# Performance work log

Measured on AMD Instinct MI355X. Metric: run time of the kernel, lower is better.

Reference implementation:

```python
import jax, jax.numpy as jnp
import numpy as np

L, N, E, H = 2048, 4, 1024, 8


def setup_inputs() -> dict:
    key = jax.random.key(0)
    ks = jax.random.split(key, 5)
    s = 0.02
    x = jax.random.normal(ks[0], (L, N, E), dtype=jnp.float32)
    Wqkv = jax.random.normal(ks[1], (H, 3 * E, E), dtype=jnp.float32) * s
    bqkv = jnp.zeros((H, 3 * E), dtype=jnp.float32)
    Wo = jax.random.normal(ks[2], (H, E, E), dtype=jnp.float32) * s
    bo = jnp.zeros((H, E), dtype=jnp.float32)
    return {"x": x, "Wqkv": Wqkv, "bqkv": bqkv, "Wo": Wo, "bo": bo}


def reference(x, Wqkv, bqkv, Wo, bo):
    # x: [L, N, E]; each of H independent single-head attentions over full E,
    # outputs summed across heads (as in the torch module).
    scale = 1.0 / jnp.sqrt(jnp.asarray(E, dtype=x.dtype))
    # joint QKV projection per head: [H, L, N, 3E]
    qkv = jnp.einsum("lne,hfe->hlnf", x, Wqkv) + bqkv[:, None, None, :]
    q, k, v = jnp.split(qkv, 3, axis=-1)  # each [H, L, N, E]
    # scores over sequence: [H, N, L, L]
    scores = jnp.einsum("hlne,hmne->hnlm", q * scale, k)
    attn = jax.nn.softmax(scores, axis=-1)
    ctx = jnp.einsum("hnlm,hmne->hlne", attn, v)  # [H, L, N, E]
    out = jnp.einsum("hlne,hfe->hlnf", ctx, Wo) + bo[:, None, None, :]
    return out.sum(axis=0)  # [L, N, E]
```

## Files before the change

### kernel.cpp

```cpp
#include <hip/hip_runtime.h>

typedef __bf16 bf16;
typedef __bf16 bf16x4 __attribute__((ext_vector_type(4)));
typedef __bf16 bf16x8 __attribute__((ext_vector_type(8)));
typedef float f32x4 __attribute__((ext_vector_type(4)));
typedef unsigned int u32;
typedef unsigned short u16;

#define CL 2048
#define CN 4
#define CE 1024
#define CH 8

__device__ __forceinline__ void gload16(const bf16* g, bf16x8* l) {
  __builtin_amdgcn_global_load_lds((const __attribute__((address_space(1))) void*)g,
                                   (__attribute__((address_space(3))) void*)l, 16, 0, 0);
}

template<int BN>
__device__ __forceinline__ void gemm_mainloop256(
    const bf16* __restrict__ Abase, const bf16* __restrict__ Bbase,
    int lda, int ldb, int nk, f32x4 (&acc)[8][BN / 64])
{
  constexpr int BJ = BN / 64;
  constexpr int BCH = BN * 4;
  __shared__ bf16x8 As[4][1024];
  __shared__ bf16x8 Bs[4][BCH];

  const int t = threadIdx.x;
  const int lane = t & 63;
  const int wid = t >> 6;
  const int wr = wid >> 2, wc = wid & 3;
  const int ln15 = lane & 15, kg = lane >> 4;

  int idxA[8], idxB[BJ];
#pragma unroll
  for (int i = 0; i < 8; ++i) {
    int row = wr * 128 + i * 16 + ln15;
    idxA[i] = row * 4 + (kg ^ ((row >> 1) & 3));
  }
#pragma unroll
  for (int j = 0; j < BJ; ++j) {
    int row = wc * (BN / 4) + j * 16 + ln15;
    idxB[j] = row * 4 + (kg ^ ((row >> 1) & 3));
  }

  const int ra0 = t >> 2;          const int ca0 = (t & 3) ^ ((ra0 >> 1) & 3);
  const int ra1 = (t + 512) >> 2;  const int ca1 = ((t + 512) & 3) ^ ((ra1 >> 1) & 3);
  const bf16* aS0 = Abase + (size_t)ra0 * lda + ca0 * 8;
  const bf16* aS1 = Abase + (size_t)ra1 * lda + ca1 * 8;
  const bf16* bS0 = Bbase + (size_t)ra0 * ldb + ca0 * 8;
  const bf16* bS1 = Bbase + (size_t)ra1 * ldb + ca1 * 8;

#pragma unroll
  for (int pt = 0; pt < 3; ++pt) {
    gload16(aS0 + pt * 32, &As[pt][t]);
    gload16(aS1 + pt * 32, &As[pt][t + 512]);
    gload16(bS0 + pt * 32, &Bs[pt][t]);
    if constexpr (BN == 256) gload16(bS1 + pt * 32, &Bs[pt][t + 512]);
  }

  for (int kt = 0; kt < nk; ++kt) {
    const int rem = nk - 1 - kt;
    if constexpr (BN == 256) {
      if (rem >= 2)      asm volatile("s_waitcnt vmcnt(8)" ::: "memory");
      else if (rem == 1) asm volatile("s_waitcnt vmcnt(4)" ::: "memory");
      else               asm volatile("s_waitcnt vmcnt(0)" ::: "memory");
    } else {
      if (rem >= 2)      asm volatile("s_waitcnt vmcnt(6)" ::: "memory");
      else if (rem == 1) asm volatile("s_waitcnt vmcnt(3)" ::: "memory");
      else               asm volatile("s_waitcnt vmcnt(0)" ::: "memory");
    }
    __builtin_amdgcn_s_barrier();

    const int buf = kt & 3;
    const int nbuf = (kt + 3) & 3;
    const bool pf = (kt + 3) < nk;
    const int ko = (kt + 3) * 32;

    if (pf) {
      gload16(aS0 + ko, &As[nbuf][t]);
      gload16(aS1 + ko, &As[nbuf][t + 512]);
    }
    bf16x8 bv[BJ], av[4];
#pragma unroll
    for (int j = 0; j < BJ; ++j) bv[j] = Bs[buf][idxB[j]];
#pragma unroll
    for (int i = 0; i < 4; ++i) av[i] = As[buf][idxA[i]];
    __builtin_amdgcn_s_setprio(1);
#pragma unroll
    for (int i = 0; i < 4; ++i)
#pragma unroll
      for (int j = 0; j < BJ; ++j)
        acc[i][j] = __builtin_amdgcn_mfma_f32_16x16x32_bf16(av[i], bv[j], acc[i][j], 0, 0, 0);
    __builtin_amdgcn_s_setprio(0);

    if (pf) {
      gload16(bS0 + ko, &Bs[nbuf][t]);
      if constexpr (BN == 256) gload16(bS1 + ko, &Bs[nbuf][t + 512]);
    }
#pragma unroll
    for (int i = 0; i < 4; ++i) av[i] = As[buf][idxA[i + 4]];
    __builtin_amdgcn_s_setprio(1);
#pragma unroll
    for (int i = 0; i < 4; ++i)
#pragma unroll
      for (int j = 0; j < BJ; ++j)
        acc[i + 4][j] = __builtin_amdgcn_mfma_f32_16x16x32_bf16(av[i], bv[j], acc[i + 4][j], 0, 0, 0);
    __builtin_amdgcn_s_setprio(0);
  }
}

__global__ void k_cast(const float4* __restrict__ in, bf16x4* __restrict__ out, int n4) {
  int i = blockIdx.x * 256 + threadIdx.x;
  if (i < n4) {
    float4 v = in[i];
    bf16x4 o = {(bf16)v.x, (bf16)v.y, (bf16)v.z, (bf16)v.w};
    out[i] = o;
  }
}

__global__ __launch_bounds__(512, 2)
void k_qkv(const bf16* __restrict__ xb, const bf16* __restrict__ Whb,
           const float* __restrict__ bqkv3,
           bf16* __restrict__ qb, bf16* __restrict__ kb, bf16* __restrict__ vb)
{
  const int bm = blockIdx.x, bn = blockIdx.y;
  f32x4 acc[8][2] = {};
  const bf16* Ab = xb + (size_t)bm * 256 * CE;
  const bf16* Bb = Whb + (size_t)bn * 128 * CE;
  gemm_mainloop256<128>(Ab, Bb, CE, CE, CE / 32, acc);

  const int lane = threadIdx.x & 63, wid = threadIdx.x >> 6;
  const int wr = wid >> 2, wc = wid & 3, ln15 = lane & 15, kg = lane >> 4;
  const int f0 = bn * 128;
  bf16* dst; int e0; float scale = 1.0f;
  if (f0 < CE)          { dst = qb; e0 = f0;          scale = 0.03125f; }
  else if (f0 < 2 * CE) { dst = kb; e0 = f0 - CE; }
  else                  { dst = vb; e0 = f0 - 2 * CE; }
#pragma unroll
  for (int i = 0; i < 8; ++i)
#pragma unroll
    for (int r = 0; r < 4; ++r) {
      int m = bm * 256 + wr * 128 + i * 16 + kg * 4 + r;
      int l = m >> 2, n = m & 3;
      size_t rowbase = ((size_t)n * CL + l) * CE;
#pragma unroll
      for (int j = 0; j < 2; ++j) {
        int fo = wc * 32 + j * 16 + ln15;
        float v = acc[i][j][r] + bqkv3[f0 + fo];
        dst[rowbase + e0 + fo] = (bf16)(v * scale);
      }
    }
}

__global__ void k_transpose(const bf16* __restrict__ v, bf16* __restrict__ vt)
{
  __shared__ u16 s[64][66];
  const bf16* src = v + (size_t)blockIdx.z * CL * CE;
  bf16* dst = vt + (size_t)blockIdx.z * CE * CL;
  const int l0 = blockIdx.x * 64, e0 = blockIdx.y * 64;
  const int t = threadIdx.x;
#pragma unroll
  for (int rr = 0; rr < 2; ++rr) {
    int c = t + rr * 256;
    int row = c >> 3, cb = (c & 7) * 8;
    uint4 d = *(const uint4*)(src + (size_t)(l0 + row) * CE + e0 + cb);
    u32* sp = (u32*)&s[row][cb];
    sp[0] = d.x; sp[1] = d.y; sp[2] = d.z; sp[3] = d.w;
  }
  __syncthreads();
  const int erow = t >> 2, lc = (t & 3) * 16;
  u32 w[8];
#pragma unroll
  for (int q = 0; q < 8; ++q) {
    u16 a = s[lc + 2 * q][erow];
    u16 b = s[lc + 2 * q + 1][erow];
    w[q] = (u32)a | ((u32)b << 16);
  }
  bf16* dp = dst + (size_t)(e0 + erow) * CL + l0 + lc;
  ((uint4*)dp)[0] = make_uint4(w[0], w[1], w[2], w[3]);
  ((uint4*)dp)[1] = make_uint4(w[4], w[5], w[6], w[7]);
}

__global__ __launch_bounds__(512, 2)
void k_scores(const bf16* __restrict__ qb, const bf16* __restrict__ kb,
              bf16* __restrict__ S)
{
  const int bm = blockIdx.x, bn = blockIdx.y, p = blockIdx.z;
  f32x4 acc[8][4] = {};
  const bf16* Ab = qb + (size_t)p * CL * CE + (size_t)bm * 256 * CE;
  const bf16* Bb = kb + (size_t)p * CL * CE + (size_t)bn * 256 * CE;
  gemm_mainloop256<256>(Ab, Bb, CE, CE, CE / 32, acc);

  const int lane = threadIdx.x & 63, wid = threadIdx.x >> 6;
  const int wr = wid >> 2, wc = wid & 3, ln15 = lane & 15, kg = lane >> 4;
  bf16* Sp = S + (size_t)p * CL * CL;
#pragma unroll
  for (int i = 0; i < 8; ++i)
#pragma unroll
    for (int r = 0; r < 4; ++r) {
      int row = bm * 256 + wr * 128 + i * 16 + kg * 4 + r;
#pragma unroll
      for (int j = 0; j < 4; ++j) {
        int col = bn * 256 + wc * 64 + j * 16 + ln15;
        Sp[(size_t)row * CL + col] = (bf16)acc[i][j][r];
      }
    }
}

__global__ __launch_bounds__(256)
void k_softmax(bf16* __restrict__ S)
{
  const int wid = threadIdx.x >> 6, lane = threadIdx.x & 63;
  const size_t row = (size_t)blockIdx.x * 4 + wid;
  ushort4* pv = (ushort4*)(S + row * CL);
  ushort4 d[8];
  float v[32];
#pragma unroll
  for (int c = 0; c < 8; ++c) d[c] = pv[c * 64 + lane];
#pragma unroll
  for (int c = 0; c < 8; ++c) {
    v[c*4+0] = __builtin_bit_cast(float, (u32)d[c].x << 16);
    v[c*4+1] = __builtin_bit_cast(float, (u32)d[c].y << 16);
    v[c*4+2] = __builtin_bit_cast(float, (u32)d[c].z << 16);
    v[c*4+3] = __builtin_bit_cast(float, (u32)d[c].w << 16);
  }
  float m = -1e30f;
#pragma unroll
  for (int i = 0; i < 32; ++i) m = fmaxf(m, v[i]);
#pragma unroll
  for (int o = 32; o; o >>= 1) m = fmaxf(m, __shfl_xor(m, o));
  float ssum = 0.f;
#pragma unroll
  for (int i = 0; i < 32; ++i) { v[i] = __expf(v[i] - m); ssum += v[i]; }
#pragma unroll
  for (int o = 32; o; o >>= 1) ssum += __shfl_xor(ssum, o);
  const float inv = 1.0f / ssum;
#pragma unroll
  for (int c = 0; c < 8; ++c) {
    ushort4 o;
    o.x = __builtin_bit_cast(u16, (bf16)(v[c*4+0] * inv));
    o.y = __builtin_bit_cast(u16, (bf16)(v[c*4+1] * inv));
    o.z = __builtin_bit_cast(u16, (bf16)(v[c*4+2] * inv));
    o.w = __builtin_bit_cast(u16, (bf16)(v[c*4+3] * inv));
    pv[c * 64 + lane] = o;
  }
}

__global__ __launch_bounds__(512, 2)
void k_pv(const bf16* __restrict__ S, const bf16* __restrict__ vt,
          bf16* __restrict__ ctx)
{
  const int bm = blockIdx.x, bn = blockIdx.y, p = blockIdx.z;
  f32x4 acc[8][2] = {};
  const bf16* Ab = S + (size_t)p * CL * CL + (size_t)bm * 256 * CL;
  const bf16* Bb = vt + (size_t)p * CE * CL + (size_t)bn * 128 * CL;
  gemm_mainloop256<128>(Ab, Bb, CL, CL, CL / 32, acc);

  const int lane = threadIdx.x & 63, wid = threadIdx.x >> 6;
  const int wr = wid >> 2, wc = wid & 3, ln15 = lane & 15, kg = lane >> 4;
#pragma unroll
  for (int i = 0; i < 8; ++i)
#pragma unroll
    for (int r = 0; r < 4; ++r) {
      int l = bm * 256 + wr * 128 + i * 16 + kg * 4 + r;
      int m = l * 4 + p;
#pragma unroll
      for (int j = 0; j < 2; ++j) {
        int e = bn * 128 + wc * 32 + j * 16 + ln15;
        ctx[(size_t)m * CE + e] = (bf16)acc[i][j][r];
      }
    }
}

__global__ __launch_bounds__(512, 2)
void k_outproj(const bf16* __restrict__ ctx, const bf16* __restrict__ Wohb,
               const float* __restrict__ boh, float* __restrict__ out, int init)
{
  const int bm = blockIdx.x, bn = blockIdx.y;
  f32x4 acc[8][2] = {};
  const bf16* Ab = ctx + (size_t)bm * 256 * CE;
  const bf16* Bb = Wohb + (size_t)bn * 128 * CE;
  gemm_mainloop256<128>(Ab, Bb, CE, CE, CE / 32, acc);

  const int lane = threadIdx.x & 63, wid = threadIdx.x >> 6;
  const int wr = wid >> 2, wc = wid & 3, ln15 = lane & 15, kg = lane >> 4;
#pragma unroll
  for (int i = 0; i < 8; ++i)
#pragma unroll
    for (int r = 0; r < 4; ++r) {
      int m = bm * 256 + wr * 128 + i * 16 + kg * 4 + r;
#pragma unroll
      for (int j = 0; j < 2; ++j) {
        int f = bn * 128 + wc * 32 + j * 16 + ln15;
        size_t idx = (size_t)m * CE + f;
        float prev = init ? 0.0f : out[idx];
        out[idx] = prev + acc[i][j][r] + boh[f];
      }
    }
}

extern "C" void kernel_launch(void* const* d_in, const int* in_sizes, int n_in,
                              void* d_out, int out_size, void* d_ws, size_t ws_size,
                              hipStream_t stream) {
  const float* x    = (const float*)d_in[0];
  const float* Wqkv = (const float*)d_in[1];
  const float* bqkv = (const float*)d_in[2];
  const float* Wo   = (const float*)d_in[3];
  const float* bo   = (const float*)d_in[4];
  float* out = (float*)d_out;

  bf16* xb   = (bf16*)d_ws;
  bf16* Whb  = xb   + (size_t)8192 * 1024;
  bf16* Wohb = Whb  + (size_t)3072 * 1024;
  bf16* qb   = Wohb + (size_t)1024 * 1024;
  bf16* kb   = qb   + (size_t)4 * 2048 * 1024;
  bf16* Sb   = kb   + (size_t)4 * 2048 * 1024;
  bf16* vtb  = Sb   + (size_t)4 * 2048 * 2048;
  bf16* vb   = Sb;
  bf16* ctx  = qb;

  const size_t needed = ((size_t)(8 + 3 + 1 + 8 + 8 + 16 + 8) * 1024 * 1024) * sizeof(bf16);
  if (ws_size < needed) return;

  k_cast<<<dim3(8192), 256, 0, stream>>>((const float4*)x, (bf16x4*)xb, 8192 * 1024 / 4);

  for (int h = 0; h < CH; ++h) {
    k_cast<<<dim3(3072), 256, 0, stream>>>((const float4*)(Wqkv + (size_t)h * 3072 * 1024),
                                           (bf16x4*)Whb, 3072 * 1024 / 4);
    k_cast<<<dim3(1024), 256, 0, stream>>>((const float4*)(Wo + (size_t)h * 1024 * 1024),
                                           (bf16x4*)Wohb, 1024 * 1024 / 4);
    k_qkv<<<dim3(32, 24), 512, 0, stream>>>(xb, Whb, bqkv + (size_t)h * 3 * CE, qb, kb, vb);
    k_transpose<<<dim3(32, 16, 4), 256, 0, stream>>>(vb, vtb);
    k_scores<<<dim3(8, 8, 4), 512, 0, stream>>>(qb, kb, Sb);
    k_softmax<<<dim3(2048), 256, 0, stream>>>(Sb);
    k_pv<<<dim3(8, 8, 4), 512, 0, stream>>>(Sb, vtb, ctx);
    k_outproj<<<dim3(32, 8), 512, 0, stream>>>(ctx, Wohb, bo + (size_t)h * CE, out, h == 0);
  }
}
```

Before: 2.109 ms.

## Use 256x256 8-phase GEMM mainloop and batch two heads per launch

Replaces the 4-stage 256x128/256x256 GEMM mainloop with a double-buffered 256x256 tile and BK=64, split into four quadrant phases that interleave LDS reads, prefetch loads and MFMA. All GEMM kernels switch to 256-wide N tiles. The host loop processes two heads per chunk when workspace allows, so each launch has twice the blocks, and the output projection accumulates both heads in registers before one read-modify-write of the output. This aims to cut launch count, output traffic and per-tile load overhead, at the cost of more workspace, more accumulator registers, and a more intricate buffer schedule.

```diff
diff --git a/kernel.cpp b/kernel.cpp
--- a/kernel.cpp
+++ b/kernel.cpp
@@ -17,99 +17,95 @@
                                    (__attribute__((address_space(3))) void*)l, 16, 0, 0);
 }
 
-template<int BN>
-__device__ __forceinline__ void gemm_mainloop256(
+__device__ __forceinline__ void gemm8p(
     const bf16* __restrict__ Abase, const bf16* __restrict__ Bbase,
-    int lda, int ldb, int nk, f32x4 (&acc)[8][BN / 64])
-{
-  constexpr int BJ = BN / 64;
-  constexpr int BCH = BN * 4;
-  __shared__ bf16x8 As[4][1024];
-  __shared__ bf16x8 Bs[4][BCH];
-
+    int lda, int ldb, int nk, f32x4 (&acc)[8][4])
+{
+  __shared__ bf16x8 Al[2][2][1024];
+  __shared__ bf16x8 Bl[2][2][1024];
   const int t = threadIdx.x;
-  const int lane = t & 63;
-  const int wid = t >> 6;
-  const int wr = wid >> 2, wc = wid & 3;
+  const int lane = t & 63, w = t >> 6;
+  const int wm = w >> 2, wn = w & 3;
   const int ln15 = lane & 15, kg = lane >> 4;
 
-  int idxA[8], idxB[BJ];
-#pragma unroll
-  for (int i = 0; i < 8; ++i) {
-    int row = wr * 128 + i * 16 + ln15;
-    idxA[i] = row * 4 + (kg ^ ((row >> 1) & 3));
-  }
-#pragma unroll
-  for (int j = 0; j < BJ; ++j) {
-    int row = wc * (BN / 4) + j * 16 + ln15;
-    idxB[j] = row * 4 + (kg ^ ((row >> 1) & 3));
-  }
-
-  const int ra0 = t >> 2;          const int ca0 = (t & 3) ^ ((ra0 >> 1) & 3);
-  const int ra1 = (t + 512) >> 2;  const int ca1 = ((t + 512) & 3) ^ ((ra1 >> 1) & 3);
-  const bf16* aS0 = Abase + (size_t)ra0 * lda + ca0 * 8;
-  const bf16* aS1 = Abase + (size_t)ra1 * lda + ca1 * 8;
-  const bf16* bS0 = Bbase + (size_t)ra0 * ldb + ca0 * 8;
-  const bf16* bS1 = Bbase + (size_t)ra1 * ldb + ca1 * 8;
-
-#pragma unroll
-  for (int pt = 0; pt < 3; ++pt) {
-    gload16(aS0 + pt * 32, &As[pt][t]);
-    gload16(aS1 + pt * 32, &As[pt][t + 512]);
-    gload16(bS0 + pt * 32, &Bs[pt][t]);
-    if constexpr (BN == 256) gload16(bS1 + pt * 32, &Bs[pt][t + 512]);
-  }
+  const int row0 = t >> 3;
+  const int cs0 = (t & 7) ^ (((t >> 5) & 1) << 1);
+  const size_t offA0 = (size_t)row0 * lda + cs0 * 8;
+  const size_t offA1 = offA0 + (size_t)64 * lda;
+  const size_t offB0 = (size_t)row0 * ldb + cs0 * 8;
+  const size_t offB1 = offB0 + (size_t)64 * ldb;
+
+  auto stA = [&](int d, int h, int tt) {
+    const bf16* g = Abase + (size_t)h * 128 * lda + tt * 64;
+    gload16(g + offA0, &Al[d][h][t]);
+    gload16(g + offA1, &Al[d][h][t + 512]);
+  };
+  auto stB = [&](int d, int h, int tt) {
+    const bf16* g = Bbase + (size_t)h * 128 * ldb + tt * 64;
+    gload16(g + offB0, &Bl[d][h][t]);
+    gload16(g + offB1, &Bl[d][h][t + 512]);
+  };
+
+  int ixA[4][2], ixB[2][2];
+#pragma unroll
+  for (int i = 0; i < 4; ++i) {
+    int r = wm * 64 + i * 16 + ln15;
+    int sw = ((r >> 2) & 1) << 1;
+#pragma unroll
+    for (int kk = 0; kk < 2; ++kk) ixA[i][kk] = r * 8 + ((kk * 4 + kg) ^ sw);
+  }
+#pragma unroll
+  for (int j = 0; j < 2; ++j) {
+    int r = wn * 32 + j * 16 + ln15;
+    int sw = ((r >> 2) & 1) << 1;
+#pragma unroll
+    for (int kk = 0; kk < 2; ++kk) ixB[j][kk] = r * 8 + ((kk * 4 + kg) ^ sw);
+  }
+
+  stA(0, 0, 0); stB(0, 0, 0); stA(0, 1, 0); stB(0, 1, 0);
+  if (nk > 1) { stA(1, 0, 1); stB(1, 1, 1); }
 
   for (int kt = 0; kt < nk; ++kt) {
-    const int rem = nk - 1 - kt;
-    if constexpr (BN == 256) {
-      if (rem >= 2)      asm volatile("s_waitcnt vmcnt(8)" ::: "memory");
-      else if (rem == 1) asm volatile("s_waitcnt vmcnt(4)" ::: "memory");
-      else               asm volatile("s_waitcnt vmcnt(0)" ::: "memory");
-    } else {
-      if (rem >= 2)      asm volatile("s_waitcnt vmcnt(6)" ::: "memory");
-      else if (rem == 1) asm volatile("s_waitcnt vmcnt(3)" ::: "memory");
-      else               asm volatile("s_waitcnt vmcnt(0)" ::: "memory");
-    }
+    const int d = kt & 1;
+    if (kt < nk - 1) asm volatile("s_waitcnt vmcnt(4)" ::: "memory");
+    else             asm volatile("s_waitcnt vmcnt(0)" ::: "memory");
     __builtin_amdgcn_s_barrier();
-
-    const int buf = kt & 3;
-    const int nbuf = (kt + 3) & 3;
-    const bool pf = (kt + 3) < nk;
-    const int ko = (kt + 3) * 32;
-
-    if (pf) {
-      gload16(aS0 + ko, &As[nbuf][t]);
-      gload16(aS1 + ko, &As[nbuf][t + 512]);
-    }
-    bf16x8 bv[BJ], av[4];
-#pragma unroll
-    for (int j = 0; j < BJ; ++j) bv[j] = Bs[buf][idxB[j]];
-#pragma unroll
-    for (int i = 0; i < 4; ++i) av[i] = As[buf][idxA[i]];
-    __builtin_amdgcn_s_setprio(1);
-#pragma unroll
-    for (int i = 0; i < 4; ++i)
-#pragma unroll
-      for (int j = 0; j < BJ; ++j)
-        acc[i][j] = __builtin_amdgcn_mfma_f32_16x16x32_bf16(av[i], bv[j], acc[i][j], 0, 0, 0);
-    __builtin_amdgcn_s_setprio(0);
-
-    if (pf) {
-      gload16(bS0 + ko, &Bs[nbuf][t]);
-      if constexpr (BN == 256) gload16(bS1 + ko, &Bs[nbuf][t + 512]);
-    }
-#pragma unroll
-    for (int i = 0; i < 4; ++i) av[i] = As[buf][idxA[i + 4]];
-    __builtin_amdgcn_s_setprio(1);
-#pragma unroll
-    for (int i = 0; i < 4; ++i)
-#pragma unroll
-      for (int j = 0; j < BJ; ++j)
-        acc[i + 4][j] = __builtin_amdgcn_mfma_f32_16x16x32_bf16(av[i], bv[j], acc[i + 4][j], 0, 0, 0);
-    __builtin_amdgcn_s_setprio(0);
-  }
-}
+#pragma unroll
+    for (int p = 0; p < 4; ++p) {
+      const int qm = p >> 1, qn = (p >> 1) ^ (p & 1);
+      bf16x8 av[4][2], bv[2][2];
+#pragma unroll
+      for (int i = 0; i < 4; ++i)
+#pragma unroll
+        for (int kk = 0; kk < 2; ++kk) av[i][kk] = Al[d][qm][ixA[i][kk]];
+#pragma unroll
+      for (int j = 0; j < 2; ++j)
+#pragma unroll
+        for (int kk = 0; kk < 2; ++kk) bv[j][kk] = Bl[d][qn][ixB[j][kk]];
+      __builtin_amdgcn_sched_barrier(0);
+      if (p == 0)      { if (kt + 1 < nk) stA(d ^ 1, 1, kt + 1); }
+      else if (p == 1) { if (kt + 1 < nk) stB(d ^ 1, 0, kt + 1); }
+      else if (p == 2) { if (kt + 2 < nk) stA(d, 0, kt + 2); }
+      else             { if (kt + 2 < nk) stB(d, 1, kt + 2); }
+      __builtin_amdgcn_s_barrier();
+      __builtin_amdgcn_s_setprio(1);
+#pragma unroll
+      for (int i = 0; i < 4; ++i)
+#pragma unroll
+        for (int j = 0; j < 2; ++j)
+#pragma unroll
+          for (int kk = 0; kk < 2; ++kk)
+            acc[qm * 4 + i][qn * 2 + j] = __builtin_amdgcn_mfma_f32_16x16x32_bf16(
+                av[i][kk], bv[j][kk], acc[qm * 4 + i][qn * 2 + j], 0, 0, 0);
+      __builtin_amdgcn_s_setprio(0);
+      __builtin_amdgcn_sched_barrier(0);
+      __builtin_amdgcn_s_barrier();
+    }
+  }
+}
+
+#define EPI_ROW(mi, r) (((mi) >> 2) * 128 + wm * 64 + ((mi) & 3) * 16 + kg * 4 + (r))
+#define EPI_COL(nj)    (((nj) >> 1) * 128 + wn * 32 + ((nj) & 1) * 16 + ln15)
 
 __global__ void k_cast(const float4* __restrict__ in, bf16x4* __restrict__ out, int n4) {
   int i = blockIdx.x * 256 + threadIdx.x;
@@ -122,33 +118,34 @@
 
 __global__ __launch_bounds__(512, 2)
 void k_qkv(const bf16* __restrict__ xb, const bf16* __restrict__ Whb,
-           const float* __restrict__ bqkv3,
+           const float* __restrict__ bqkvc,
            bf16* __restrict__ qb, bf16* __restrict__ kb, bf16* __restrict__ vb)
 {
-  const int bm = blockIdx.x, bn = blockIdx.y;
-  f32x4 acc[8][2] = {};
+  const int bm = blockIdx.x, bn = blockIdx.y, z = blockIdx.z;
+  f32x4 acc[8][4] = {};
   const bf16* Ab = xb + (size_t)bm * 256 * CE;
-  const bf16* Bb = Whb + (size_t)bn * 128 * CE;
-  gemm_mainloop256<128>(Ab, Bb, CE, CE, CE / 32, acc);
-
-  const int lane = threadIdx.x & 63, wid = threadIdx.x >> 6;
-  const int wr = wid >> 2, wc = wid & 3, ln15 = lane & 15, kg = lane >> 4;
-  const int f0 = bn * 128;
+  const bf16* Bb = Whb + (size_t)z * 3 * CE * CE + (size_t)bn * 256 * CE;
+  gemm8p(Ab, Bb, CE, CE, CE / 64, acc);
+
+  const int lane = threadIdx.x & 63, w = threadIdx.x >> 6;
+  const int wm = w >> 2, wn = w & 3, ln15 = lane & 15, kg = lane >> 4;
+  const int f0 = bn * 256;
+  const float* bias = bqkvc + (size_t)z * 3 * CE;
   bf16* dst; int e0; float scale = 1.0f;
   if (f0 < CE)          { dst = qb; e0 = f0;          scale = 0.03125f; }
   else if (f0 < 2 * CE) { dst = kb; e0 = f0 - CE; }
   else                  { dst = vb; e0 = f0 - 2 * CE; }
 #pragma unroll
-  for (int i = 0; i < 8; ++i)
+  for (int mi = 0; mi < 8; ++mi)
 #pragma unroll
     for (int r = 0; r < 4; ++r) {
-      int m = bm * 256 + wr * 128 + i * 16 + kg * 4 + r;
+      int m = bm * 256 + EPI_ROW(mi, r);
       int l = m >> 2, n = m & 3;
-      size_t rowbase = ((size_t)n * CL + l) * CE;
-#pragma unroll
-      for (int j = 0; j < 2; ++j) {
-        int fo = wc * 32 + j * 16 + ln15;
-        float v = acc[i][j][r] + bqkv3[f0 + fo];
+      size_t rowbase = ((size_t)(z * 4 + n) * CL + l) * CE;
+#pragma unroll
+      for (int nj = 0; nj < 4; ++nj) {
+        int fo = EPI_COL(nj);
+        float v = acc[mi][nj][r] + bias[f0 + fo];
         dst[rowbase + e0 + fo] = (bf16)(v * scale);
       }
     }
@@ -171,16 +168,16 @@
   }
   __syncthreads();
   const int erow = t >> 2, lc = (t & 3) * 16;
-  u32 w[8];
+  u32 wv[8];
 #pragma unroll
   for (int q = 0; q < 8; ++q) {
     u16 a = s[lc + 2 * q][erow];
     u16 b = s[lc + 2 * q + 1][erow];
-    w[q] = (u32)a | ((u32)b << 16);
+    wv[q] = (u32)a | ((u32)b << 16);
   }
   bf16* dp = dst + (size_t)(e0 + erow) * CL + l0 + lc;
-  ((uint4*)dp)[0] = make_uint4(w[0], w[1], w[2], w[3]);
-  ((uint4*)dp)[1] = make_uint4(w[4], w[5], w[6], w[7]);
+  ((uint4*)dp)[0] = make_uint4(wv[0], wv[1], wv[2], wv[3]);
+  ((uint4*)dp)[1] = make_uint4(wv[4], wv[5], wv[6], wv[7]);
 }
 
 __global__ __launch_bounds__(512, 2)
@@ -191,20 +188,20 @@
   f32x4 acc[8][4] = {};
   const bf16* Ab = qb + (size_t)p * CL * CE + (size_t)bm * 256 * CE;
   const bf16* Bb = kb + (size_t)p * CL * CE + (size_t)bn * 256 * CE;
-  gemm_mainloop256<256>(Ab, Bb, CE, CE, CE / 32, acc);
-
-  const int lane = threadIdx.x & 63, wid = threadIdx.x >> 6;
-  const int wr = wid >> 2, wc = wid & 3, ln15 = lane & 15, kg = lane >> 4;
+  gemm8p(Ab, Bb, CE, CE, CE / 64, acc);
+
+  const int lane = threadIdx.x & 63, w = threadIdx.x >> 6;
+  const int wm = w >> 2, wn = w & 3, ln15 = lane & 15, kg = lane >> 4;
   bf16* Sp = S + (size_t)p * CL * CL;
 #pragma unroll
-  for (int i = 0; i < 8; ++i)
+  for (int mi = 0; mi < 8; ++mi)
 #pragma unroll
     for (int r = 0; r < 4; ++r) {
-      int row = bm * 256 + wr * 128 + i * 16 + kg * 4 + r;
-#pragma unroll
-      for (int j = 0; j < 4; ++j) {
-        int col = bn * 256 + wc * 64 + j * 16 + ln15;
-        Sp[(size_t)row * CL + col] = (bf16)acc[i][j][r];
+      int row = bm * 256 + EPI_ROW(mi, r);
+#pragma unroll
+      for (int nj = 0; nj < 4; ++nj) {
+        int col = bn * 256 + EPI_COL(nj);
+        Sp[(size_t)row * CL + col] = (bf16)acc[mi][nj][r];
       }
     }
 }
@@ -253,50 +250,56 @@
           bf16* __restrict__ ctx)
 {
   const int bm = blockIdx.x, bn = blockIdx.y, p = blockIdx.z;
-  f32x4 acc[8][2] = {};
+  f32x4 acc[8][4] = {};
   const bf16* Ab = S + (size_t)p * CL * CL + (size_t)bm * 256 * CL;
-  const bf16* Bb = vt + (size_t)p * CE * CL + (size_t)bn * 128 * CL;
-  gemm_mainloop256<128>(Ab, Bb, CL, CL, CL / 32, acc);
-
-  const int lane = threadIdx.x & 63, wid = threadIdx.x >> 6;
-  const int wr = wid >> 2, wc = wid & 3, ln15 = lane & 15, kg = lane >> 4;
-#pragma unroll
-  for (int i = 0; i < 8; ++i)
+  const bf16* Bb = vt + (size_t)p * CE * CL + (size_t)bn * 256 * CL;
+  gemm8p(Ab, Bb, CL, CL, CL / 64, acc);
+
+  const int lane = threadIdx.x & 63, w = threadIdx.x >> 6;
+  const int wm = w >> 2, wn = w & 3, ln15 = lane & 15, kg = lane >> 4;
+  const int hl = p >> 2, n = p & 3;
+  bf16* cp = ctx + (size_t)hl * (CL * CN) * CE;
+#pragma unroll
+  for (int mi = 0; mi < 8; ++mi)
 #pragma unroll
     for (int r = 0; r < 4; ++r) {
-      int l = bm * 256 + wr * 128 + i * 16 + kg * 4 + r;
-      int m = l * 4 + p;
-#pragma unroll
-      for (int j = 0; j < 2; ++j) {
-        int e = bn * 128 + wc * 32 + j * 16 + ln15;
-        ctx[(size_t)m * CE + e] = (bf16)acc[i][j][r];
+      int l = bm * 256 + EPI_ROW(mi, r);
+      int m = l * 4 + n;
+#pragma unroll
+      for (int nj = 0; nj < 4; ++nj) {
+        int e = bn * 256 + EPI_COL(nj);
+        cp[(size_t)m * CE + e] = (bf16)acc[mi][nj][r];
       }
     }
 }
 
 __global__ __launch_bounds__(512, 2)
 void k_outproj(const bf16* __restrict__ ctx, const bf16* __restrict__ Wohb,
-               const float* __restrict__ boh, float* __restrict__ out, int init)
+               const float* __restrict__ boc, float* __restrict__ out,
+               int chunk, int init)
 {
   const int bm = blockIdx.x, bn = blockIdx.y;
-  f32x4 acc[8][2] = {};
-  const bf16* Ab = ctx + (size_t)bm * 256 * CE;
-  const bf16* Bb = Wohb + (size_t)bn * 128 * CE;
-  gemm_mainloop256<128>(Ab, Bb, CE, CE, CE / 32, acc);
-
-  const int lane = threadIdx.x & 63, wid = threadIdx.x >> 6;
-  const int wr = wid >> 2, wc = wid & 3, ln15 = lane & 15, kg = lane >> 4;
-#pragma unroll
-  for (int i = 0; i < 8; ++i)
+  f32x4 acc[8][4] = {};
+  for (int hl = 0; hl < chunk; ++hl) {
+    const bf16* Ab = ctx + ((size_t)hl * (CL * CN) + (size_t)bm * 256) * CE;
+    const bf16* Bb = Wohb + ((size_t)hl * CE + (size_t)bn * 256) * CE;
+    gemm8p(Ab, Bb, CE, CE, CE / 64, acc);
+  }
+  const int lane = threadIdx.x & 63, w = threadIdx.x >> 6;
+  const int wm = w >> 2, wn = w & 3, ln15 = lane & 15, kg = lane >> 4;
+#pragma unroll
+  for (int mi = 0; mi < 8; ++mi)
 #pragma unroll
     for (int r = 0; r < 4; ++r) {
-      int m = bm * 256 + wr * 128 + i * 16 + kg * 4 + r;
-#pragma unroll
-      for (int j = 0; j < 2; ++j) {
-        int f = bn * 128 + wc * 32 + j * 16 + ln15;
+      int m = bm * 256 + EPI_ROW(mi, r);
+#pragma unroll
+      for (int nj = 0; nj < 4; ++nj) {
+        int f = bn * 256 + EPI_COL(nj);
+        float bsum = 0.f;
+        for (int hl = 0; hl < chunk; ++hl) bsum += boc[hl * CE + f];
         size_t idx = (size_t)m * CE + f;
         float prev = init ? 0.0f : out[idx];
-        out[idx] = prev + acc[i][j][r] + boh[f];
+        out[idx] = prev + acc[mi][nj][r] + bsum;
       }
     }
 }
@@ -311,31 +314,40 @@
   const float* bo   = (const float*)d_in[4];
   float* out = (float*)d_out;
 
+  const size_t Me = 1024 * 1024;
+  auto need = [&](int ch) {
+    return (size_t)(8 + ch * (3 + 1 + 8 + 8 + 16 + 8)) * Me * sizeof(bf16);
+  };
+  int chunk = (ws_size >= need(2)) ? 2 : 1;
+  if (ws_size < need(1)) return;
+  const int P = chunk * 4;
+
   bf16* xb   = (bf16*)d_ws;
-  bf16* Whb  = xb   + (size_t)8192 * 1024;
-  bf16* Wohb = Whb  + (size_t)3072 * 1024;
-  bf16* qb   = Wohb + (size_t)1024 * 1024;
-  bf16* kb   = qb   + (size_t)4 * 2048 * 1024;
-  bf16* Sb   = kb   + (size_t)4 * 2048 * 1024;
-  bf16* vtb  = Sb   + (size_t)4 * 2048 * 2048;
+  bf16* Whb  = xb   + (size_t)8 * Me;
+  bf16* Wohb = Whb  + (size_t)chunk * 3 * Me;
+  bf16* qb   = Wohb + (size_t)chunk * 1 * Me;
+  bf16* kb   = qb   + (size_t)chunk * 8 * Me;
+  bf16* Sb   = kb   + (size_t)chunk * 8 * Me;
+  bf16* vtb  = Sb   + (size_t)chunk * 16 * Me;
   bf16* vb   = Sb;
   bf16* ctx  = qb;
 
-  const size_t needed = ((size_t)(8 + 3 + 1 + 8 + 8 + 16 + 8) * 1024 * 1024) * sizeof(bf16);
-  if (ws_size < needed) return;
-
   k_cast<<<dim3(8192), 256, 0, stream>>>((const float4*)x, (bf16x4*)xb, 8192 * 1024 / 4);
 
-  for (int h = 0; h < CH; ++h) {
-    k_cast<<<dim3(3072), 256, 0, stream>>>((const float4*)(Wqkv + (size_t)h * 3072 * 1024),
-                                           (bf16x4*)Whb, 3072 * 1024 / 4);
-    k_cast<<<dim3(1024), 256, 0, stream>>>((const float4*)(Wo + (size_t)h * 1024 * 1024),
-                                           (bf16x4*)Wohb, 1024 * 1024 / 4);
-    k_qkv<<<dim3(32, 24), 512, 0, stream>>>(xb, Whb, bqkv + (size_t)h * 3 * CE, qb, kb, vb);
-    k_transpose<<<dim3(32, 16, 4), 256, 0, stream>>>(vb, vtb);
-    k_scores<<<dim3(8, 8, 4), 512, 0, stream>>>(qb, kb, Sb);
-    k_softmax<<<dim3(2048), 256, 0, stream>>>(Sb);
-    k_pv<<<dim3(8, 8, 4), 512, 0, stream>>>(Sb, vtb, ctx);
-    k_outproj<<<dim3(32, 8), 512, 0, stream>>>(ctx, Wohb, bo + (size_t)h * CE, out, h == 0);
-  }
-}
+  for (int c = 0; c < CH / chunk; ++c) {
+    k_cast<<<dim3(chunk * 3072), 256, 0, stream>>>(
+        (const float4*)(Wqkv + (size_t)c * chunk * 3072 * 1024),
+        (bf16x4*)Whb, chunk * 3072 * 1024 / 4);
+    k_cast<<<dim3(chunk * 1024), 256, 0, stream>>>(
+        (const float4*)(Wo + (size_t)c * chunk * 1024 * 1024),
+        (bf16x4*)Wohb, chunk * 1024 * 1024 / 4);
+    k_qkv<<<dim3(32, 12, chunk), 512, 0, stream>>>(
+        xb, Whb, bqkv + (size_t)c * chunk * 3 * CE, qb, kb, vb);
+    k_transpose<<<dim3(32, 16, P), 256, 0, stream>>>(vb, vtb);
+    k_scores<<<dim3(8, 8, P), 512, 0, stream>>>(qb, kb, Sb);
+    k_softmax<<<dim3(P * 512), 256, 0, stream>>>(Sb);
+    k_pv<<<dim3(8, 4, P), 512, 0, stream>>>(Sb, vtb, ctx);
+    k_outproj<<<dim3(32, 4), 512, 0, stream>>>(
+        ctx, Wohb, bo + (size_t)c * chunk * CE, out, chunk, c == 0);
+  }
+}
```

Measured after the change: 2.121 ms. Within noise of the previous version (+0.6%).
